# Performance work log

Measured on AMD Instinct MI355X. Metric: run time of the kernel, lower is better.

The kernel has to match this reference:

```python
import jax, jax.numpy as jnp
import numpy as np

B, ND, NS, V, D, H, N, NL = 1024, 13, 26, 10000, 64, 8, 16, 4
SEQ = 1 + ND + NS  # cls + dense fields + sparse fields = 40


def _ln(x, g, b):
    m = x.mean(-1, keepdims=True)
    v = x.var(-1, keepdims=True)
    return (x - m) / jnp.sqrt(v + 1e-5) * g + b


def _mamba(x, g, b, xW, xb, A, Dp, oW, ob):
    # Faithful to MambaBlock: normed x feeds proj, state, and D-skip; residual is pre-norm x.
    xn = _ln(x, g, b)
    xp = xn @ xW.T + xb                              # (B,L,2D)
    delta, Bm = jnp.split(xp, 2, axis=-1)
    delta = jax.nn.softplus(delta)
    # h in torch is (B,L,D,1); (h*A_disc).sum(-1) == h * sum_n exp(delta*A[:,n])
    gate = jnp.exp(delta[..., None] * A).sum(-1)     # (B,L,D)
    h = jnp.cumsum(xn * Bm, axis=1)                  # (B,L,D)
    out = h * gate + xn * Dp
    return out @ oW.T + ob + x


def _fwd(dense_x, dense_W, dense_b, embed_tables, cls_token, mb_norm_g, mb_norm_b, mb_xproj_W, mb_xproj_b, mb_A, mb_D, mb_out_W, mb_out_b, merge_W, merge_b, attn_in_W, attn_in_b, attn_out_W, attn_out_b, mlp_W1, mlp_b1, mlp_W2, mlp_b2, mlp_W3, mlp_b3, sparse_idx):
    Bsz = dense_x.shape[0]
    dense_emb = (dense_x @ dense_W.T + dense_b).reshape(Bsz, ND, D)
    idx = jnp.clip(sparse_idx, 0, V)                 # clamp(0, num_embeddings-1)
    sparse_emb = embed_tables[jnp.arange(NS)[None, :], idx]   # (B,NS,D)
    seq = jnp.concatenate([jnp.broadcast_to(cls_token, (Bsz, 1, D)), dense_emb, sparse_emb], axis=1)
    for i in range(NL):
        f = _mamba(seq, mb_norm_g[i, 0], mb_norm_b[i, 0], mb_xproj_W[i, 0], mb_xproj_b[i, 0], mb_A[i, 0], mb_D[i, 0], mb_out_W[i, 0], mb_out_b[i, 0])
        r = _mamba(seq[:, ::-1], mb_norm_g[i, 1], mb_norm_b[i, 1], mb_xproj_W[i, 1], mb_xproj_b[i, 1], mb_A[i, 1], mb_D[i, 1], mb_out_W[i, 1], mb_out_b[i, 1])[:, ::-1]
        seq = jnp.concatenate([f, r], axis=-1) @ merge_W[i].T + merge_b[i]
    # nn.MultiheadAttention (batch_first, eval): packed qkv proj, scaled dot-product, out proj
    qkv = seq @ attn_in_W.T + attn_in_b
    q, k, v = jnp.split(qkv, 3, axis=-1)
    hd = D // H
    rs = lambda t: t.reshape(Bsz, SEQ, H, hd).transpose(0, 2, 1, 3)
    q, k, v = rs(q), rs(k), rs(v)
    att = jax.nn.softmax(jnp.einsum('bhqd,bhkd->bhqk', q, k) / float(np.sqrt(hd)), axis=-1)
    ao = jnp.einsum('bhqk,bhkd->bhqd', att, v).transpose(0, 2, 1, 3).reshape(Bsz, SEQ, D)
    seq = seq + ao @ attn_out_W.T + attn_out_b
    c = seq[:, 0]
    h1 = jax.nn.relu(c @ mlp_W1.T + mlp_b1)
    h2 = jax.nn.relu(h1 @ mlp_W2.T + mlp_b2)
    return (h2 @ mlp_W3.T + mlp_b3)[:, 0]


def setup_inputs():
    ks = iter(jax.random.split(jax.random.key(0), 64))
    nrm = lambda shape, s=0.02: jax.random.normal(next(ks), shape, jnp.float32) * s
    inp = {}
    inp['dense_x'] = jax.random.normal(next(ks), (B, ND), jnp.float32)
    inp['dense_W'] = nrm((ND * D, ND)); inp['dense_b'] = jnp.zeros((ND * D,), jnp.float32)
    tbl = nrm((NS, V + 1, D)); inp['embed_tables'] = tbl.at[:, 0, :].set(0.0)  # padding_idx=0
    inp['cls_token'] = nrm((1, 1, D))
    inp['mb_norm_g'] = jnp.ones((NL, 2, D), jnp.float32); inp['mb_norm_b'] = jnp.zeros((NL, 2, D), jnp.float32)
    inp['mb_xproj_W'] = nrm((NL, 2, 2 * D, D)); inp['mb_xproj_b'] = jnp.zeros((NL, 2, 2 * D), jnp.float32)
    inp['mb_A'] = jax.random.uniform(next(ks), (NL, 2, D, N), jnp.float32, -0.01, 0.01)
    inp['mb_D'] = jnp.ones((NL, 2, D), jnp.float32)
    inp['mb_out_W'] = nrm((NL, 2, D, D)); inp['mb_out_b'] = jnp.zeros((NL, 2, D), jnp.float32)
    inp['merge_W'] = nrm((NL, D, 2 * D)); inp['merge_b'] = jnp.zeros((NL, D), jnp.float32)
    inp['attn_in_W'] = nrm((3 * D, D)); inp['attn_in_b'] = jnp.zeros((3 * D,), jnp.float32)
    inp['attn_out_W'] = nrm((D, D)); inp['attn_out_b'] = jnp.zeros((D,), jnp.float32)
    inp['mlp_W1'] = nrm((128, D)); inp['mlp_b1'] = jnp.zeros((128,), jnp.float32)
    inp['mlp_W2'] = nrm((64, 128)); inp['mlp_b2'] = jnp.zeros((64,), jnp.float32)
    inp['mlp_W3'] = nrm((1, 64)); inp['mlp_b3'] = jnp.zeros((1,), jnp.float32)
    inp['sparse_x'] = jax.random.randint(next(ks), (B, NS), 0, V, jnp.int32)
    return inp


def reference(dense_x, dense_W, dense_b, embed_tables, cls_token, mb_norm_g, mb_norm_b, mb_xproj_W, mb_xproj_b, mb_A, mb_D, mb_out_W, mb_out_b, merge_W, merge_b, attn_in_W, attn_in_b, attn_out_W, attn_out_b, mlp_W1, mlp_b1, mlp_W2, mlp_b2, mlp_W3, mlp_b3, sparse_x):
    return _fwd(dense_x, dense_W, dense_b, embed_tables, cls_token, mb_norm_g, mb_norm_b, mb_xproj_W, mb_xproj_b, mb_A, mb_D, mb_out_W, mb_out_b, merge_W, merge_b, attn_in_W, attn_in_b, attn_out_W, attn_out_b, mlp_W1, mlp_b1, mlp_W2, mlp_b2, mlp_W3, mlp_b3, sparse_x)
```

## Files before the change

### kernel.cpp

```cpp
#include <hip/hip_runtime.h>

#define DEV static __device__ __forceinline__

typedef __attribute__((ext_vector_type(8))) short bf16x8;
typedef __attribute__((ext_vector_type(4))) float f32x4;

#define MFMA(a, b, c) __builtin_amdgcn_mfma_f32_16x16x32_bf16(a, b, c, 0, 0, 0)

DEV float bf2f(unsigned short h) { return __uint_as_float(((unsigned)h) << 16); }
DEV unsigned short f2bf(float f) {
  unsigned u = __float_as_uint(f);
  u += 0x7fffu + ((u >> 16) & 1u);
  return (unsigned short)(u >> 16);
}
DEV bf16x8 ld8(const unsigned short* p) { return *(const bf16x8*)p; }

DEV float dotg64(const float* x, const float* wrow) {
  const float4* wp = (const float4*)wrow;
  float a0 = 0.f, a1 = 0.f;
  #pragma unroll
  for (int c = 0; c < 8; ++c) {
    float4 u = wp[2*c], v = wp[2*c + 1];
    a0 = fmaf(u.x, x[8*c+0], a0); a0 = fmaf(u.y, x[8*c+1], a0);
    a0 = fmaf(u.z, x[8*c+2], a0); a0 = fmaf(u.w, x[8*c+3], a0);
    a1 = fmaf(v.x, x[8*c+4], a1); a1 = fmaf(v.y, x[8*c+5], a1);
    a1 = fmaf(v.z, x[8*c+6], a1); a1 = fmaf(v.w, x[8*c+7], a1);
  }
  return a0 + a1;
}
DEV float wred64(float v) {
  #pragma unroll
  for (int o = 32; o > 0; o >>= 1) v += __shfl_xor(v, o, 64);
  return v;
}

#define XW_HI 0
#define XW_LO 65536
#define CW 131072
#define AI_HI 262144
#define AI_LO 274432
#define SC_OFF 286720
#define BP_OFF 290816


__global__ void prep_kernel(const float* __restrict__ xW, const float* __restrict__ oW,
                            const float* __restrict__ ob, const float* __restrict__ mW,
                            const float* __restrict__ mb, const float* __restrict__ aiW,
                            const float* __restrict__ Ap, unsigned short* __restrict__ wsb) {
  const int gid = blockIdx.x * blockDim.x + threadIdx.x;
  const int stride = gridDim.x * blockDim.x;
  for (int i = gid; i < 65536; i += stride) {
    float x = xW[i]; unsigned short h = f2bf(x);
    wsb[XW_HI + i] = h; wsb[XW_LO + i] = f2bf(x - bf2f(h));
  }
  for (int i = gid; i < 32768; i += stride) {
    int L = i >> 13, rem = i & 8191;
    int dir = rem >> 12, n = (rem >> 6) & 63, d = rem & 63;
    const float* mrow = mW + L*8192 + n*128 + dir*64;
    const float* ocol = oW + L*8192 + dir*4096 + d;
    float acc = 0.f;
    #pragma unroll 8
    for (int j = 0; j < 64; ++j) acc = fmaf(mrow[j], ocol[j*64], acc);
    unsigned short h = f2bf(acc);
    int base = CW + L*24576 + dir*8192;
    wsb[base + n*64 + d] = h;
    wsb[base + 4096 + n*64 + d] = f2bf(acc - bf2f(h));
  }
  for (int i = gid; i < 16384; i += stride) {
    int L = i >> 12, n = (i >> 6) & 63, j = i & 63;
    float v = mW[L*8192 + n*128 + j] + mW[L*8192 + n*128 + 64 + j];
    unsigned short h = f2bf(v);
    int base = CW + L*24576 + 16384;
    wsb[base + n*64 + j] = h;
    wsb[base + 4096 + n*64 + j] = f2bf(v - bf2f(h));
  }
  {
    float* bp = (float*)(wsb + BP_OFF);
    for (int i = gid; i < 256; i += stride) {
      int L = i >> 6, n = i & 63;
      const float* mrow = mW + L*8192 + n*128;
      float acc = mb[L*64 + n];
      #pragma unroll 8
      for (int j = 0; j < 64; ++j) acc = fmaf(ob[(2*L)*64 + j], mrow[j], acc);
      #pragma unroll 8
      for (int j = 0; j < 64; ++j) acc = fmaf(ob[(2*L+1)*64 + j], mrow[64 + j], acc);
      bp[i] = acc;
    }
  }
  for (int i = gid; i < 12288; i += stride) {
    float x = aiW[i]; unsigned short h = f2bf(x);
    wsb[AI_HI + i] = h; wsb[AI_LO + i] = f2bf(x - bf2f(h));
  }
  float* sc = (float*)(wsb + SC_OFF);
  for (int i = gid; i < 512; i += stride) {
    int pi = i >> 6, d = i & 63;
    const float* a = Ap + (size_t)i * 16;
    float s1 = 0, s2 = 0, s3 = 0, s4 = 0;
    #pragma unroll
    for (int n = 0; n < 16; ++n) {
      float z = a[n]; float z2 = z * z;
      s1 += z; s2 += z2; s3 += z2 * z; s4 += z2 * z2;
    }
    sc[pi*256 + d]       = s1;
    sc[pi*256 + 64 + d]  = s2 * 0.5f;
    sc[pi*256 + 128 + d] = s3 * (1.f/6.f);
    sc[pi*256 + 192 + d] = s4 * (1.f/24.f);
  }
}

__global__ __launch_bounds__(512, 2)
void Mamba4CTRV15_kernel(
    const float* __restrict__ dense_x, const float* __restrict__ dense_W,
    const float* __restrict__ dense_b, const float* __restrict__ tbl,
    const float* __restrict__ cls, const float* __restrict__ ng,
    const float* __restrict__ nb, const float* __restrict__ xb,
    const float* __restrict__ Dp, const float* __restrict__ ob,
    const float* __restrict__ mb, const float* __restrict__ aib,
    const float* __restrict__ aoW, const float* __restrict__ aob,
    const float* __restrict__ w1, const float* __restrict__ b1,
    const float* __restrict__ w2, const float* __restrict__ b2,
    const float* __restrict__ w3, const float* __restrict__ b3,
    const int* __restrict__ sidx, const unsigned short* __restrict__ wsb,
    float* __restrict__ out) {
  __shared__ __align__(16) unsigned char smem[145408];
  float*          s_seq  = (float*)smem;
  unsigned short* s_xnb  = (unsigned short*)(smem + 40960);
  unsigned short* bG0    = (unsigned short*)(smem + 61440);
  unsigned short* bG1    = (unsigned short*)(smem + 81920);
  unsigned short* bB0    = (unsigned short*)(smem + 102400);
  unsigned short* bB1    = (unsigned short*)(smem + 122880);
  float*          s_small= (float*)(smem + 143360);
  float* g0f = (float*)bG0;
  float* g1f = (float*)bG1;
  const float* scf = (const float*)(wsb + SC_OFF);
  const float* bpf = (const float*)(wsb + BP_OFF);

  const int tid = threadIdx.x, b = blockIdx.x;
  const int lane = tid & 63, wv = tid >> 6;
  const int arow = lane & 15;
  const int aq = (lane >> 4) * 8;
  const int rq = (lane >> 4) * 4;
  const int rq7 = rq & 7;
  const int swA = (arow & 7) << 3;
  const int aqs0 = aq ^ swA, aqs1 = (aq + 32) ^ swA;

  {
    float* s_dx = s_small;
    int* s_idx = (int*)(s_small + 64);
    if (tid < 64) {
      int br = tid >> 4, k = tid & 15;
      if (k < 13) s_dx[tid] = dense_x[(b*4 + br)*13 + k];
    }
    if (tid >= 64 && tid < 168) {
      int s = tid - 64, br = s / 26, si = s - br*26;
      int v = sidx[(b*4 + br)*26 + si];
      v = v < 0 ? 0 : (v > 10000 ? 10000 : v);
      s_idx[s] = v;
    }
    __syncthreads();
    if (tid < 256) s_seq[(tid >> 6)*40*64 + (tid & 63)] = cls[tid & 63];
    {
      const int br = tid >> 7, j0 = tid & 127;
      float x[13];
      #pragma unroll
      for (int k = 0; k < 13; ++k) x[k] = s_dx[br*16 + k];
      for (int j = j0; j < 832; j += 128) {
        float acc = dense_b[j];
        #pragma unroll
        for (int k = 0; k < 13; ++k) acc = fmaf(x[k], dense_W[j*13 + k], acc);
        s_seq[(br*40 + 1 + (j >> 6))*64 + (j & 63)] = acc;
      }
    }
    for (int e = tid; e < 1664; e += 512) {
      int br = e / 416, rem = e - br*416, s = rem >> 4, c = rem & 15;
      const float4* row = (const float4*)(tbl + ((size_t)(s*10001 + s_idx[br*26 + s]))*64);
      ((float4*)&s_seq[(br*40 + 14 + s)*64])[c] = row[c];
    }
  }
  __syncthreads();

  for (int L = 0; L < 4; ++L) {
    const int pi0 = 2*L, pi1 = 2*L + 1;

    {
      const int g = lane >> 4, dl = lane & 15;
      const int dbase = 4 * ((dl + 4*g) & 15);
      const float4 ngv = *(const float4*)&ng[pi0*64 + dbase];
      const float4 nbv = *(const float4*)&nb[pi0*64 + dbase];
      #pragma unroll 1
      for (int sweep = 0; sweep < 5; ++sweep) {
        int t = sweep*32 + wv*4 + g;
        const float4 xv = *(const float4*)&s_seq[t*64 + dbase];
        float s = (xv.x + xv.y) + (xv.z + xv.w);
        float q = fmaf(xv.x, xv.x, fmaf(xv.y, xv.y, fmaf(xv.z, xv.z, xv.w*xv.w)));
        #pragma unroll
        for (int o = 8; o > 0; o >>= 1) { s += __shfl_xor(s, o, 64); q += __shfl_xor(q, o, 64); }
        float mean = s * (1.f/64.f);
        float var = q * (1.f/64.f) - mean*mean;
        float rs = rsqrtf(var + 1e-5f);
        unsigned short h0 = f2bf(fmaf((xv.x - mean)*rs, ngv.x, nbv.x));
        unsigned short h1 = f2bf(fmaf((xv.y - mean)*rs, ngv.y, nbv.y));
        unsigned short h2 = f2bf(fmaf((xv.z - mean)*rs, ngv.z, nbv.z));
        unsigned short h3 = f2bf(fmaf((xv.w - mean)*rs, ngv.w, nbv.w));
        int o2 = (t << 6) + (dbase ^ ((t & 7) << 3));
        unsigned lo = (unsigned)h0 | ((unsigned)h1 << 16);
        unsigned hi = (unsigned)h2 | ((unsigned)h3 << 16);
        *(uint2*)&s_xnb[o2] = make_uint2(lo, hi);
      }
    }
    __syncthreads();

    {
      const int j = wv*16 + arow;
      const unsigned short* Wh0 = wsb + XW_HI + pi0*8192 + j*64;
      const unsigned short* Wl0 = wsb + XW_LO + pi0*8192 + j*64;
      const unsigned short* Wh1 = wsb + XW_HI + pi1*8192 + j*64;
      const unsigned short* Wl1 = wsb + XW_LO + pi1*8192 + j*64;
      bf16x8 bh00 = ld8(Wh0 + aq), bh01 = ld8(Wh0 + 32 + aq);
      bf16x8 bl00 = ld8(Wl0 + aq), bl01 = ld8(Wl0 + 32 + aq);
      bf16x8 bh10 = ld8(Wh1 + aq), bh11 = ld8(Wh1 + 32 + aq);
      bf16x8 bl10 = ld8(Wl1 + aq), bl11 = ld8(Wl1 + 32 + aq);
      const float bj0 = xb[pi0*128 + j], bj1 = xb[pi1*128 + j];
      const bool isDelta = (wv < 4);
      float c10=0,c20=0,c30=0,c40=0,c11=0,c21=0,c31=0,c41=0;
      if (isDelta) {
        c10=scf[pi0*256+j]; c20=scf[pi0*256+64+j]; c30=scf[pi0*256+128+j]; c40=scf[pi0*256+192+j];
        c11=scf[pi1*256+j]; c21=scf[pi1*256+64+j]; c31=scf[pi1*256+128+j]; c41=scf[pi1*256+192+j];
      }
      #pragma unroll 1
      for (int mt = 0; mt < 10; ++mt) {
        const unsigned short* A = s_xnb + ((mt*16 + arow) << 6);
        bf16x8 ah0 = ld8(A + aqs0), ah1 = ld8(A + aqs1);
        f32x4 a0 = {0,0,0,0}, a1 = {0,0,0,0};
        a0 = MFMA(ah0, bh00, a0); a0 = MFMA(ah0, bl00, a0);
        a0 = MFMA(ah1, bh01, a0); a0 = MFMA(ah1, bl01, a0);
        a1 = MFMA(ah0, bh10, a1); a1 = MFMA(ah0, bl10, a1);
        a1 = MFMA(ah1, bh11, a1); a1 = MFMA(ah1, bl11, a1);
        const int rbase = mt*16 + rq;
        #pragma unroll
        for (int r = 0; r < 4; ++r) {
          int row = rbase + r;
          int swr = (rq7 + r) << 3;
          float x0v = a0[r] + bj0, x1v = a1[r] + bj1;
          if (isDelta) {
            float sp0 = fmaxf(x0v, 0.f) + __logf(1.f + __expf(-fabsf(x0v)));
            float sp1 = fmaxf(x1v, 0.f) + __logf(1.f + __expf(-fabsf(x1v)));
            int o = (row << 6) + (j ^ swr);
            bG0[o] = f2bf(sp0 * fmaf(sp0, fmaf(sp0, fmaf(sp0, c40, c30), c20), c10));
            bG1[o] = f2bf(sp1 * fmaf(sp1, fmaf(sp1, fmaf(sp1, c41, c31), c21), c11));
          } else {
            int o = (row << 6) + ((j - 64) ^ swr);
            bB0[o] = f2bf(x0v);
            bB1[o] = f2bf(x1v);
          }
        }
      }
    }
    __syncthreads();

    if (tid < 256) {
      const int d0 = (tid & 31) * 2, br = (tid >> 5) & 3, dir = tid >> 7;
      unsigned short* bmb = dir ? bB1 : bB0;
      unsigned short* gb = dir ? bG1 : bG0;
      const float2 dpd = *(const float2*)&Dp[(pi0 + dir)*64 + d0];
      const int base = br*40;
      float run0 = 0.f, run1 = 0.f;
      #pragma unroll
      for (int k = 0; k < 40; ++k) {
        int t = base + (dir ? (39 - k) : k);
        int o = (t << 6) + (d0 ^ ((t & 7) << 3));
        unsigned xn2 = *(const unsigned*)&s_xnb[o];
        unsigned bm2 = *(const unsigned*)&bmb[o];
        unsigned g2  = *(const unsigned*)&gb[o];
        float xn0 = bf2f((unsigned short)xn2), xn1 = bf2f((unsigned short)(xn2 >> 16));
        run0 = fmaf(xn0, bf2f((unsigned short)bm2), run0);
        run1 = fmaf(xn1, bf2f((unsigned short)(bm2 >> 16)), run1);
        float gate0 = 16.f + bf2f((unsigned short)g2);
        float gate1 = 16.f + bf2f((unsigned short)(g2 >> 16));
        unsigned short r0 = f2bf(fmaf(run0, gate0, xn0 * dpd.x));
        unsigned short r1 = f2bf(fmaf(run1, gate1, xn1 * dpd.y));
        *(unsigned*)&gb[o] = (unsigned)r0 | ((unsigned)r1 << 16);
        if (dir == 0) {
          float2 sv = *(const float2*)&s_seq[t*64 + d0];
          *(unsigned*)&bmb[o] = (unsigned)f2bf(sv.x) | ((unsigned)f2bf(sv.y) << 16);
        }
      }
    }
    __syncthreads();

    {
      const int n0 = (wv & 3)*16 + arow;
      const int mt0 = (wv < 4) ? 0 : 5, mt1 = (wv < 4) ? 5 : 10;
      const unsigned short* cbase = wsb + CW + L*24576;
      const unsigned short* C0H = cbase + n0*64;
      const unsigned short* C0L = cbase + 4096 + n0*64;
      const unsigned short* C1H = cbase + 8192 + n0*64;
      const unsigned short* C1L = cbase + 12288 + n0*64;
      const unsigned short* SH  = cbase + 16384 + n0*64;
      const unsigned short* SL  = cbase + 20480 + n0*64;
      bf16x8 c0h0 = ld8(C0H + aq), c0h1 = ld8(C0H + 32 + aq);
      bf16x8 c0l0 = ld8(C0L + aq), c0l1 = ld8(C0L + 32 + aq);
      bf16x8 c1h0 = ld8(C1H + aq), c1h1 = ld8(C1H + 32 + aq);
      bf16x8 c1l0 = ld8(C1L + aq), c1l1 = ld8(C1L + 32 + aq);
      bf16x8 sh0 = ld8(SH + aq), sh1 = ld8(SH + 32 + aq);
      bf16x8 sl0 = ld8(SL + aq), sl1 = ld8(SL + 32 + aq);
      const float bom = bpf[L*64 + n0];
      #pragma unroll 1
      for (int mt = mt0; mt < mt1; ++mt) {
        const unsigned short* A0 = bG0 + ((mt*16 + arow) << 6);
        const unsigned short* A1 = bG1 + ((mt*16 + arow) << 6);
        const unsigned short* AR = bB0 + ((mt*16 + arow) << 6);
        bf16x8 g00 = ld8(A0 + aqs0), g01 = ld8(A0 + aqs1);
        bf16x8 g10 = ld8(A1 + aqs0), g11 = ld8(A1 + aqs1);
        bf16x8 r0 = ld8(AR + aqs0), r1 = ld8(AR + aqs1);
        f32x4 a0 = {0,0,0,0}, a1 = {0,0,0,0}, a2 = {0,0,0,0};
        a0 = MFMA(g00, c0h0, a0); a0 = MFMA(g00, c0l0, a0);
        a0 = MFMA(g01, c0h1, a0); a0 = MFMA(g01, c0l1, a0);
        a1 = MFMA(g10, c1h0, a1); a1 = MFMA(g10, c1l0, a1);
        a1 = MFMA(g11, c1h1, a1); a1 = MFMA(g11, c1l1, a1);
        a2 = MFMA(r0, sh0, a2); a2 = MFMA(r0, sl0, a2);
        a2 = MFMA(r1, sh1, a2); a2 = MFMA(r1, sl1, a2);
        const int rbase = mt*16 + rq;
        #pragma unroll
        for (int r = 0; r < 4; ++r) {
          int row = rbase + r;
          float v = a0[r] + a1[r] + a2[r] + bom;
          s_seq[row*64 + n0] = v;
          if (L == 3) s_xnb[(row << 6) + (n0 ^ ((rq7 + r) << 3))] = f2bf(v);
        }
      }
    }
    __syncthreads();
  }

  {
    #pragma unroll 1
    for (int i = 0; i < 12; ++i) {
      const int u = wv + 8*i;
      int j, mtk;
      if (u < 80) { j = 64 + (u & 7)*16 + arow; mtk = u >> 3; }
      else {
        int qi = u - 80;
        j = (qi & 3)*16 + arow;
        int p = qi >> 2;
        mtk = p*2 + (p >> 1);
      }
      const unsigned short* Wh = wsb + AI_HI + j*64;
      const unsigned short* Wl = wsb + AI_LO + j*64;
      bf16x8 bh0 = ld8(Wh + aq), bh1 = ld8(Wh + 32 + aq);
      bf16x8 bl0 = ld8(Wl + aq), bl1 = ld8(Wl + 32 + aq);
      const float bj = aib[j];
      const unsigned short* A = s_xnb + ((mtk*16 + arow) << 6);
      bf16x8 ah0 = ld8(A + aqs0), ah1 = ld8(A + aqs1);
      f32x4 a0 = {0,0,0,0};
      a0 = MFMA(ah0, bh0, a0); a0 = MFMA(ah0, bl0, a0);
      a0 = MFMA(ah1, bh1, a0); a0 = MFMA(ah1, bl1, a0);
      const int rbase = mtk*16 + rq;
      #pragma unroll
      for (int r = 0; r < 4; ++r) {
        int row = rbase + r;
        int swr = (rq7 + r) << 3;
        float val = a0[r] + bj;
        if (u < 80) {
          if (j < 128) bB0[(row << 6) + ((j - 64) ^ swr)] = f2bf(val);
          else         bB1[(row << 6) + ((j - 128) ^ swr)] = f2bf(val);
        } else {
          if (row % 40 == 0) g0f[(row/40)*720 + 320 + j] = val;
        }
      }
    }
    if (tid < 256) g0f[(tid >> 6)*720 + 384 + (tid & 63)] = s_seq[(tid >> 6)*40*64 + (tid & 63)];
  }
  __syncthreads();

  for (int e = tid; e < 1280; e += 512) {
    int br = e / 320, rem = e - br*320;
    int h = rem / 40, kk = rem - h*40;
    int row = br*40 + kk;
    int kbase = (row << 6) + ((h*8) ^ ((kk & 7) << 3));
    float acc = 0.f;
    #pragma unroll
    for (int i = 0; i < 8; ++i)
      acc += g0f[br*720 + 320 + h*8 + i] * bf2f(bB0[kbase + i]);
    g0f[br*720 + rem] = acc * 0.35355339059327373f;
  }
  __syncthreads();

  {
    const int hh = wv*4 + (lane >> 4), jl = lane & 15;
    float* pr = g0f + (hh >> 3)*720 + (hh & 7)*40;
    float a = pr[jl];
    float bv = pr[16 + jl];
    float cv = (jl < 8) ? pr[32 + jl] : -1e30f;
    float m = fmaxf(fmaxf(a, bv), cv);
    #pragma unroll
    for (int o = 8; o > 0; o >>= 1) m = fmaxf(m, __shfl_xor(m, o, 16));
    float pa = __expf(a - m), pb = __expf(bv - m), pc = (jl < 8) ? __expf(cv - m) : 0.f;
    float s = pa + pb + pc;
    #pragma unroll
    for (int o = 8; o > 0; o >>= 1) s += __shfl_xor(s, o, 16);
    float inv = 1.f / s;
    pr[jl] = pa * inv;
    pr[16 + jl] = pb * inv;
    if (jl < 8) pr[32 + jl] = pc * inv;
  }
  __syncthreads();

  for (int e = tid; e < 1024; e += 512) {
    const int d = e & 63, qrt = (e >> 6) & 3, br = e >> 8, hh = d >> 3;
    float acc = 0.f;
    #pragma unroll
    for (int k = qrt*10; k < qrt*10 + 10; ++k) {
      int o = ((br*40 + k) << 6) + (d ^ ((k & 7) << 3));
      acc += g0f[br*720 + hh*40 + k] * bf2f(bB1[o]);
    }
    g1f[br*512 + qrt*64 + d] = acc;
  }
  __syncthreads();
  if (tid < 256) {
    float* p = g1f + (tid >> 6)*512;
    int d = tid & 63;
    p[256 + d] = p[d] + p[64 + d] + p[128 + d] + p[192 + d];
  }
  __syncthreads();

  if (tid < 256) {
    int br = tid >> 6, o = tid & 63;
    g0f[br*720 + 448 + o] = g0f[br*720 + 384 + o] + aob[o]
                          + dotg64(&g1f[br*512 + 256], aoW + (size_t)o*64);
  }
  __syncthreads();

  {
    int br = tid >> 7, o = tid & 127;
    g1f[br*512 + 320 + o] = fmaxf(b1[o] + dotg64(&g0f[br*720 + 448], w1 + (size_t)o*64), 0.f);
  }
  __syncthreads();

  if (tid < 256) {
    int br = tid >> 6, o = tid & 63;
    float acc = dotg64(&g1f[br*512 + 320], w2 + (size_t)o*128)
              + dotg64(&g1f[br*512 + 384], w2 + (size_t)o*128 + 64);
    g1f[br*512 + 448 + o] = fmaxf(acc + b2[o], 0.f);
  }
  __syncthreads();

  if (tid < 256) {
    int br = tid >> 6;
    float v = g1f[br*512 + 448 + lane] * w3[lane];
    v = wred64(v);
    if (lane == 0) out[b*4 + br] = v + b3[0];
  }
}

extern "C" void kernel_launch(void* const* d_in, const int* in_sizes, int n_in,
                              void* d_out, int out_size, void* d_ws, size_t ws_size,
                              hipStream_t stream) {
  (void)n_in; (void)ws_size; (void)out_size;
  const float* dense_x = (const float*)d_in[0];
  const float* dense_W = (const float*)d_in[1];
  const float* dense_b = (const float*)d_in[2];
  const float* tbl     = (const float*)d_in[3];
  const float* cls     = (const float*)d_in[4];
  const float* ng      = (const float*)d_in[5];
  const float* nb      = (const float*)d_in[6];
  const float* xW      = (const float*)d_in[7];
  const float* xb      = (const float*)d_in[8];
  const float* Ap      = (const float*)d_in[9];
  const float* Dp      = (const float*)d_in[10];
  const float* oW      = (const float*)d_in[11];
  const float* ob      = (const float*)d_in[12];
  const float* mW      = (const float*)d_in[13];
  const float* mb      = (const float*)d_in[14];
  const float* aiW     = (const float*)d_in[15];
  const float* aib     = (const float*)d_in[16];
  const float* aoW     = (const float*)d_in[17];
  const float* aob     = (const float*)d_in[18];
  const float* w1      = (const float*)d_in[19];
  const float* b1      = (const float*)d_in[20];
  const float* w2      = (const float*)d_in[21];
  const float* b2      = (const float*)d_in[22];
  const float* w3      = (const float*)d_in[23];
  const float* b3      = (const float*)d_in[24];
  const int*   sidx    = (const int*)d_in[25];
  float* out = (float*)d_out;
  unsigned short* wsb = (unsigned short*)d_ws;

  hipLaunchKernelGGL(prep_kernel, dim3(256), dim3(256), 0, stream,
                     xW, oW, ob, mW, mb, aiW, Ap, wsb);

  const int B = in_sizes[0] / 13;
  hipLaunchKernelGGL(Mamba4CTRV15_kernel, dim3(B/4), dim3(512), 0, stream,
                     dense_x, dense_W, dense_b, tbl, cls, ng, nb, xb, Dp, ob, mb,
                     aib, aoW, aob, w1, b1, w2, b2, w3, b3, sidx, wsb, out);
}
```

Measured before the change: 254.8 us.

## Process two batch rows per block with 256 threads instead of four with 512

Halves the per-block work from four samples to two, shrinking the block to 256 threads and the shared-memory footprint from about 142KB to 70KB, and doubles the grid size. Each wave now covers two column tiles in the projection GEMM and all row tiles in the merge step, and the work-index mappings are remapped to match. The intent is more resident blocks per CU and finer-grained scheduling across CUs. The cost is that per-block weight fragments are loaded from global memory for fewer samples, so weight traffic per sample roughly doubles.

```diff
diff --git a/kernel.cpp b/kernel.cpp
--- a/kernel.cpp
+++ b/kernel.cpp
@@ -108,8 +108,8 @@
   }
 }
 
-__global__ __launch_bounds__(512, 2)
-void Mamba4CTRV15_kernel(
+__global__ __launch_bounds__(256, 2)
+void Mamba4CTRV16_kernel(
     const float* __restrict__ dense_x, const float* __restrict__ dense_W,
     const float* __restrict__ dense_b, const float* __restrict__ tbl,
     const float* __restrict__ cls, const float* __restrict__ ng,
@@ -122,14 +122,13 @@
     const float* __restrict__ w3, const float* __restrict__ b3,
     const int* __restrict__ sidx, const unsigned short* __restrict__ wsb,
     float* __restrict__ out) {
-  __shared__ __align__(16) unsigned char smem[145408];
+  __shared__ __align__(16) unsigned char smem[71680];
   float*          s_seq  = (float*)smem;
-  unsigned short* s_xnb  = (unsigned short*)(smem + 40960);
-  unsigned short* bG0    = (unsigned short*)(smem + 61440);
-  unsigned short* bG1    = (unsigned short*)(smem + 81920);
-  unsigned short* bB0    = (unsigned short*)(smem + 102400);
-  unsigned short* bB1    = (unsigned short*)(smem + 122880);
-  float*          s_small= (float*)(smem + 143360);
+  unsigned short* s_xnb  = (unsigned short*)(smem + 20480);
+  unsigned short* bG0    = (unsigned short*)(smem + 30720);
+  unsigned short* bG1    = (unsigned short*)(smem + 40960);
+  unsigned short* bB0    = (unsigned short*)(smem + 51200);
+  unsigned short* bB1    = (unsigned short*)(smem + 61440);
   float* g0f = (float*)bG0;
   float* g1f = (float*)bG1;
   const float* scf = (const float*)(wsb + SC_OFF);
@@ -145,20 +144,18 @@
   const int aqs0 = aq ^ swA, aqs1 = (aq + 32) ^ swA;
 
   {
-    float* s_dx = s_small;
-    int* s_idx = (int*)(s_small + 64);
-    if (tid < 64) {
-      int br = tid >> 4, k = tid & 15;
-      if (k < 13) s_dx[tid] = dense_x[(b*4 + br)*13 + k];
-    }
-    if (tid >= 64 && tid < 168) {
+    float* s_dx = g0f;
+    int* s_idx = (int*)(g0f + 32);
+    if (tid < 13) s_dx[tid] = dense_x[(b*2)*13 + tid];
+    else if (tid >= 16 && tid < 29) s_dx[tid] = dense_x[(b*2+1)*13 + (tid-16)];
+    if (tid >= 64 && tid < 116) {
       int s = tid - 64, br = s / 26, si = s - br*26;
-      int v = sidx[(b*4 + br)*26 + si];
+      int v = sidx[(b*2+br)*26 + si];
       v = v < 0 ? 0 : (v > 10000 ? 10000 : v);
       s_idx[s] = v;
     }
     __syncthreads();
-    if (tid < 256) s_seq[(tid >> 6)*40*64 + (tid & 63)] = cls[tid & 63];
+    if (tid < 128) s_seq[(tid >> 6)*40*64 + (tid & 63)] = cls[tid & 63];
     {
       const int br = tid >> 7, j0 = tid & 127;
       float x[13];
@@ -171,7 +168,7 @@
         s_seq[(br*40 + 1 + (j >> 6))*64 + (j & 63)] = acc;
       }
     }
-    for (int e = tid; e < 1664; e += 512) {
+    for (int e = tid; e < 832; e += 256) {
       int br = e / 416, rem = e - br*416, s = rem >> 4, c = rem & 15;
       const float4* row = (const float4*)(tbl + ((size_t)(s*10001 + s_idx[br*26 + s]))*64);
       ((float4*)&s_seq[(br*40 + 14 + s)*64])[c] = row[c];
@@ -189,7 +186,7 @@
       const float4 nbv = *(const float4*)&nb[pi0*64 + dbase];
       #pragma unroll 1
       for (int sweep = 0; sweep < 5; ++sweep) {
-        int t = sweep*32 + wv*4 + g;
+        int t = sweep*16 + wv*4 + g;
         const float4 xv = *(const float4*)&s_seq[t*64 + dbase];
         float s = (xv.x + xv.y) + (xv.z + xv.w);
         float q = fmaf(xv.x, xv.x, fmaf(xv.y, xv.y, fmaf(xv.z, xv.z, xv.w*xv.w)));
@@ -211,55 +208,58 @@
     __syncthreads();
 
     {
-      const int j = wv*16 + arow;
-      const unsigned short* Wh0 = wsb + XW_HI + pi0*8192 + j*64;
-      const unsigned short* Wl0 = wsb + XW_LO + pi0*8192 + j*64;
-      const unsigned short* Wh1 = wsb + XW_HI + pi1*8192 + j*64;
-      const unsigned short* Wl1 = wsb + XW_LO + pi1*8192 + j*64;
-      bf16x8 bh00 = ld8(Wh0 + aq), bh01 = ld8(Wh0 + 32 + aq);
-      bf16x8 bl00 = ld8(Wl0 + aq), bl01 = ld8(Wl0 + 32 + aq);
-      bf16x8 bh10 = ld8(Wh1 + aq), bh11 = ld8(Wh1 + 32 + aq);
-      bf16x8 bl10 = ld8(Wl1 + aq), bl11 = ld8(Wl1 + 32 + aq);
-      const float bj0 = xb[pi0*128 + j], bj1 = xb[pi1*128 + j];
-      const bool isDelta = (wv < 4);
-      float c10=0,c20=0,c30=0,c40=0,c11=0,c21=0,c31=0,c41=0;
-      if (isDelta) {
-        c10=scf[pi0*256+j]; c20=scf[pi0*256+64+j]; c30=scf[pi0*256+128+j]; c40=scf[pi0*256+192+j];
-        c11=scf[pi1*256+j]; c21=scf[pi1*256+64+j]; c31=scf[pi1*256+128+j]; c41=scf[pi1*256+192+j];
-      }
       #pragma unroll 1
-      for (int mt = 0; mt < 10; ++mt) {
-        const unsigned short* A = s_xnb + ((mt*16 + arow) << 6);
-        bf16x8 ah0 = ld8(A + aqs0), ah1 = ld8(A + aqs1);
-        f32x4 a0 = {0,0,0,0}, a1 = {0,0,0,0};
-        a0 = MFMA(ah0, bh00, a0); a0 = MFMA(ah0, bl00, a0);
-        a0 = MFMA(ah1, bh01, a0); a0 = MFMA(ah1, bl01, a0);
-        a1 = MFMA(ah0, bh10, a1); a1 = MFMA(ah0, bl10, a1);
-        a1 = MFMA(ah1, bh11, a1); a1 = MFMA(ah1, bl11, a1);
-        const int rbase = mt*16 + rq;
-        #pragma unroll
-        for (int r = 0; r < 4; ++r) {
-          int row = rbase + r;
-          int swr = (rq7 + r) << 3;
-          float x0v = a0[r] + bj0, x1v = a1[r] + bj1;
-          if (isDelta) {
-            float sp0 = fmaxf(x0v, 0.f) + __logf(1.f + __expf(-fabsf(x0v)));
-            float sp1 = fmaxf(x1v, 0.f) + __logf(1.f + __expf(-fabsf(x1v)));
-            int o = (row << 6) + (j ^ swr);
-            bG0[o] = f2bf(sp0 * fmaf(sp0, fmaf(sp0, fmaf(sp0, c40, c30), c20), c10));
-            bG1[o] = f2bf(sp1 * fmaf(sp1, fmaf(sp1, fmaf(sp1, c41, c31), c21), c11));
-          } else {
-            int o = (row << 6) + ((j - 64) ^ swr);
-            bB0[o] = f2bf(x0v);
-            bB1[o] = f2bf(x1v);
+      for (int cti = 0; cti < 2; ++cti) {
+        const int j = (wv + cti*4)*16 + arow;
+        const unsigned short* Wh0 = wsb + XW_HI + pi0*8192 + j*64;
+        const unsigned short* Wl0 = wsb + XW_LO + pi0*8192 + j*64;
+        const unsigned short* Wh1 = wsb + XW_HI + pi1*8192 + j*64;
+        const unsigned short* Wl1 = wsb + XW_LO + pi1*8192 + j*64;
+        bf16x8 bh00 = ld8(Wh0 + aq), bh01 = ld8(Wh0 + 32 + aq);
+        bf16x8 bl00 = ld8(Wl0 + aq), bl01 = ld8(Wl0 + 32 + aq);
+        bf16x8 bh10 = ld8(Wh1 + aq), bh11 = ld8(Wh1 + 32 + aq);
+        bf16x8 bl10 = ld8(Wl1 + aq), bl11 = ld8(Wl1 + 32 + aq);
+        const float bj0 = xb[pi0*128 + j], bj1 = xb[pi1*128 + j];
+        const bool isDelta = (cti == 0);
+        float c10=0,c20=0,c30=0,c40=0,c11=0,c21=0,c31=0,c41=0;
+        if (isDelta) {
+          c10=scf[pi0*256+j]; c20=scf[pi0*256+64+j]; c30=scf[pi0*256+128+j]; c40=scf[pi0*256+192+j];
+          c11=scf[pi1*256+j]; c21=scf[pi1*256+64+j]; c31=scf[pi1*256+128+j]; c41=scf[pi1*256+192+j];
+        }
+        #pragma unroll 1
+        for (int mt = 0; mt < 5; ++mt) {
+          const unsigned short* A = s_xnb + ((mt*16 + arow) << 6);
+          bf16x8 ah0 = ld8(A + aqs0), ah1 = ld8(A + aqs1);
+          f32x4 a0 = {0,0,0,0}, a1 = {0,0,0,0};
+          a0 = MFMA(ah0, bh00, a0); a0 = MFMA(ah0, bl00, a0);
+          a0 = MFMA(ah1, bh01, a0); a0 = MFMA(ah1, bl01, a0);
+          a1 = MFMA(ah0, bh10, a1); a1 = MFMA(ah0, bl10, a1);
+          a1 = MFMA(ah1, bh11, a1); a1 = MFMA(ah1, bl11, a1);
+          const int rbase = mt*16 + rq;
+          #pragma unroll
+          for (int r = 0; r < 4; ++r) {
+            int row = rbase + r;
+            int swr = (rq7 + r) << 3;
+            float x0v = a0[r] + bj0, x1v = a1[r] + bj1;
+            if (isDelta) {
+              float sp0 = fmaxf(x0v, 0.f) + __logf(1.f + __expf(-fabsf(x0v)));
+              float sp1 = fmaxf(x1v, 0.f) + __logf(1.f + __expf(-fabsf(x1v)));
+              int o = (row << 6) + (j ^ swr);
+              bG0[o] = f2bf(sp0 * fmaf(sp0, fmaf(sp0, fmaf(sp0, c40, c30), c20), c10));
+              bG1[o] = f2bf(sp1 * fmaf(sp1, fmaf(sp1, fmaf(sp1, c41, c31), c21), c11));
+            } else {
+              int o = (row << 6) + ((j - 64) ^ swr);
+              bB0[o] = f2bf(x0v);
+              bB1[o] = f2bf(x1v);
+            }
           }
         }
       }
     }
     __syncthreads();
 
-    if (tid < 256) {
-      const int d0 = (tid & 31) * 2, br = (tid >> 5) & 3, dir = tid >> 7;
+    if (tid < 128) {
+      const int d0 = (tid & 31) * 2, br = (tid >> 5) & 1, dir = tid >> 6;
       unsigned short* bmb = dir ? bB1 : bB0;
       unsigned short* gb = dir ? bG1 : bG0;
       const float2 dpd = *(const float2*)&Dp[(pi0 + dir)*64 + d0];
@@ -289,8 +289,7 @@
     __syncthreads();
 
     {
-      const int n0 = (wv & 3)*16 + arow;
-      const int mt0 = (wv < 4) ? 0 : 5, mt1 = (wv < 4) ? 5 : 10;
+      const int n0 = wv*16 + arow;
       const unsigned short* cbase = wsb + CW + L*24576;
       const unsigned short* C0H = cbase + n0*64;
       const unsigned short* C0L = cbase + 4096 + n0*64;
@@ -306,7 +305,7 @@
       bf16x8 sl0 = ld8(SL + aq), sl1 = ld8(SL + 32 + aq);
       const float bom = bpf[L*64 + n0];
       #pragma unroll 1
-      for (int mt = mt0; mt < mt1; ++mt) {
+      for (int mt = 0; mt < 5; ++mt) {
         const unsigned short* A0 = bG0 + ((mt*16 + arow) << 6);
         const unsigned short* A1 = bG1 + ((mt*16 + arow) << 6);
         const unsigned short* AR = bB0 + ((mt*16 + arow) << 6);
@@ -336,15 +335,10 @@
   {
     #pragma unroll 1
     for (int i = 0; i < 12; ++i) {
-      const int u = wv + 8*i;
+      const int u = wv + 4*i;
       int j, mtk;
-      if (u < 80) { j = 64 + (u & 7)*16 + arow; mtk = u >> 3; }
-      else {
-        int qi = u - 80;
-        j = (qi & 3)*16 + arow;
-        int p = qi >> 2;
-        mtk = p*2 + (p >> 1);
-      }
+      if (u < 40) { j = 64 + (u & 7)*16 + arow; mtk = u >> 3; }
+      else { int qi = u - 40; j = (qi & 3)*16 + arow; mtk = (qi >> 2) * 2; }
       const unsigned short* Wh = wsb + AI_HI + j*64;
       const unsigned short* Wl = wsb + AI_LO + j*64;
       bf16x8 bh0 = ld8(Wh + aq), bh1 = ld8(Wh + 32 + aq);
@@ -361,19 +355,20 @@
         int row = rbase + r;
         int swr = (rq7 + r) << 3;
         float val = a0[r] + bj;
-        if (u < 80) {
+        if (u < 40) {
           if (j < 128) bB0[(row << 6) + ((j - 64) ^ swr)] = f2bf(val);
           else         bB1[(row << 6) + ((j - 128) ^ swr)] = f2bf(val);
         } else {
-          if (row % 40 == 0) g0f[(row/40)*720 + 320 + j] = val;
+          if (row == 0)       g0f[320 + j] = val;
+          else if (row == 40) g0f[720 + 320 + j] = val;
         }
       }
     }
-    if (tid < 256) g0f[(tid >> 6)*720 + 384 + (tid & 63)] = s_seq[(tid >> 6)*40*64 + (tid & 63)];
-  }
-  __syncthreads();
-
-  for (int e = tid; e < 1280; e += 512) {
+    if (tid < 128) g0f[(tid >> 6)*720 + 384 + (tid & 63)] = s_seq[(tid >> 6)*40*64 + (tid & 63)];
+  }
+  __syncthreads();
+
+  for (int e = tid; e < 640; e += 256) {
     int br = e / 320, rem = e - br*320;
     int h = rem / 40, kk = rem - h*40;
     int row = br*40 + kk;
@@ -406,7 +401,7 @@
   }
   __syncthreads();
 
-  for (int e = tid; e < 1024; e += 512) {
+  for (int e = tid; e < 512; e += 256) {
     const int d = e & 63, qrt = (e >> 6) & 3, br = e >> 8, hh = d >> 3;
     float acc = 0.f;
     #pragma unroll
@@ -417,14 +412,14 @@
     g1f[br*512 + qrt*64 + d] = acc;
   }
   __syncthreads();
-  if (tid < 256) {
+  if (tid < 128) {
     float* p = g1f + (tid >> 6)*512;
     int d = tid & 63;
     p[256 + d] = p[d] + p[64 + d] + p[128 + d] + p[192 + d];
   }
   __syncthreads();
 
-  if (tid < 256) {
+  if (tid < 128) {
     int br = tid >> 6, o = tid & 63;
     g0f[br*720 + 448 + o] = g0f[br*720 + 384 + o] + aob[o]
                           + dotg64(&g1f[br*512 + 256], aoW + (size_t)o*64);
@@ -437,7 +432,7 @@
   }
   __syncthreads();
 
-  if (tid < 256) {
+  if (tid < 128) {
     int br = tid >> 6, o = tid & 63;
     float acc = dotg64(&g1f[br*512 + 320], w2 + (size_t)o*128)
               + dotg64(&g1f[br*512 + 384], w2 + (size_t)o*128 + 64);
@@ -445,11 +440,11 @@
   }
   __syncthreads();
 
-  if (tid < 256) {
+  if (tid < 128) {
     int br = tid >> 6;
     float v = g1f[br*512 + 448 + lane] * w3[lane];
     v = wred64(v);
-    if (lane == 0) out[b*4 + br] = v + b3[0];
+    if (lane == 0) out[b*2 + br] = v + b3[0];
   }
 }
 
@@ -490,7 +485,7 @@
                      xW, oW, ob, mW, mb, aiW, Ap, wsb);
 
   const int B = in_sizes[0] / 13;
-  hipLaunchKernelGGL(Mamba4CTRV15_kernel, dim3(B/4), dim3(512), 0, stream,
+  hipLaunchKernelGGL(Mamba4CTRV16_kernel, dim3(B/2), dim3(256), 0, stream,
                      dense_x, dense_W, dense_b, tbl, cls, ng, nb, xb, Dp, ob, mb,
                      aib, aoW, aob, w1, b1, w2, b2, w3, b3, sidx, wsb, out);
 }
```

Result: faster. 247.3 us (-2.9%).
